# Kernel tuning notes

Measured on AMD Instinct MI355X. Metric: run time of the kernel, lower is better.

The kernel has to match this reference:

```python
import jax, jax.numpy as jnp
import numpy as np

N = 8192  # source points
M = 8192  # target points
T = 8     # RL path steps


def setup_inputs() -> dict:
    key = jax.random.key(0)
    ks = jax.random.split(key, 6)
    return {
        "source": jax.random.normal(ks[0], (N, 3), jnp.float32),
        "target": jax.random.normal(ks[1], (M, 3), jnp.float32),
        "label": jax.random.uniform(ks[2], (N,), jnp.float32),
        "trans_m": 0.01 * jax.random.normal(ks[3], (T, N, 3), jnp.float32),
        "path_m": jax.random.uniform(ks[4], (T, N), jnp.float32),
        "path_maxprob_m": jax.random.uniform(ks[5], (T, N), jnp.float32, minval=0.05, maxval=1.0),
    }


def _catculate_loss2(p1, p2):
    # p1: [N,3], p2: [M,3] -> pairwise squared distances [N,M]
    dist = jnp.sum((p1[:, None, :] - p2[None, :, :]) ** 2, axis=-1)
    dist_min = jnp.min(dist, axis=-1)
    dist_max = jnp.max(dist, axis=-1)
    return 0.99 * dist_min + 0.01 * dist_max  # [N]


def reference(source, target, label, trans_m, path_m, path_maxprob_m):
    p = 0.002
    L0 = 0.4
    lammda = 0.05
    gamma = 0.99
    Tn = path_m.shape[0]

    trans_end = trans_m[-1]
    points_denoise = source - trans_end
    loss_start = _catculate_loss2(source, target)
    loss_end = _catculate_loss2(points_denoise, target)
    loss_dt = loss_end - loss_start

    d = jnp.minimum(loss_end / L0, 1.0)  # where(d>1, 1, d)
    l = jnp.exp(-label)

    reward_end = -p * path_m[-1] - (d + lammda * l) * loss_dt  # [N]
    # rewards: [N, T] = per-step path penalties then final reward
    rewards = jnp.concatenate([(-p * path_m[:-1]).T, reward_end[:, None]], axis=-1)

    logp = jnp.log(path_maxprob_m)  # [T, N]

    # discounted return scan, iterating i = T-1 .. 0
    def step(carry, xs):
        R, L = carry
        lp, r = xs
        R = gamma * R + lp * (r + 0.02)
        return (R, L - R), None

    init = (jnp.zeros_like(reward_end), jnp.zeros_like(reward_end))
    (_, L), _ = jax.lax.scan(step, init, (logp[::-1], rewards.T[::-1]))
    loss = L / Tn  # [N]
    return jnp.mean(loss)
```

## Files before the change

### kernel.cpp

```cpp
#include <hip/hip_runtime.h>
#include <math.h>

#define TPB 256
#define TILE 128

__global__ __launch_bounds__(TPB) void k1_partial_minmax(
    const float* __restrict__ source,
    const float* __restrict__ target,
    const float* __restrict__ trans_m,
    float4* __restrict__ part,
    int* __restrict__ counter,
    int N, int M, int T, int S)
{
    if (blockIdx.x == 0 && blockIdx.y == 0 && threadIdx.x == 0) *counter = 0;

    const int chunk = M / S;
    const int i = blockIdx.x * TPB + threadIdx.x;
    const int s = blockIdx.y;

    __shared__ float4 tgt[TILE];

    const float sx = source[i * 3 + 0];
    const float sy = source[i * 3 + 1];
    const float sz = source[i * 3 + 2];
    const long teoff = (long)(T - 1) * N * 3 + (long)i * 3;
    const float ex = sx - trans_m[teoff + 0];
    const float ey = sy - trans_m[teoff + 1];
    const float ez = sz - trans_m[teoff + 2];

    const float ss = fmaf(sx, sx, fmaf(sy, sy, sz * sz));
    const float ee = fmaf(ex, ex, fmaf(ey, ey, ez * ez));
    const float vsx = -2.0f * sx, vsy = -2.0f * sy, vsz = -2.0f * sz;
    const float vex = -2.0f * ex, vey = -2.0f * ey, vez = -2.0f * ez;

    float mins = 3.402823e38f, maxs = -3.402823e38f;
    float mine = 3.402823e38f, maxe = -3.402823e38f;

    const int t_begin = s * chunk;
    const int t_end   = t_begin + chunk;

    for (int t0 = t_begin; t0 < t_end; t0 += TILE) {
        __syncthreads();
        for (int j = threadIdx.x; j < TILE; j += TPB) {
            const float tx = target[(long)(t0 + j) * 3 + 0];
            const float ty = target[(long)(t0 + j) * 3 + 1];
            const float tz = target[(long)(t0 + j) * 3 + 2];
            const float q  = fmaf(tx, tx, fmaf(ty, ty, tz * tz));
            tgt[j] = make_float4(tx, ty, tz, q);
        }
        __syncthreads();

        #pragma unroll 8
        for (int j = 0; j < TILE; ++j) {
            const float4 t = tgt[j];
            float a = fmaf(vsx, t.x, t.w);
            a = fmaf(vsy, t.y, a);
            a = fmaf(vsz, t.z, a);
            mins = fminf(mins, a);
            maxs = fmaxf(maxs, a);
            float b = fmaf(vex, t.x, t.w);
            b = fmaf(vey, t.y, b);
            b = fmaf(vez, t.z, b);
            mine = fminf(mine, b);
            maxe = fmaxf(maxe, b);
        }
    }

    part[(long)s * N + i] = make_float4(mins + ss, maxs + ss, mine + ee, maxe + ee);
}

__global__ __launch_bounds__(TPB) void k2_loss(
    const float4* __restrict__ part,
    const float* __restrict__ label,
    const float* __restrict__ path_m,
    const float* __restrict__ path_maxprob_m,
    float* __restrict__ blocksums,
    int* __restrict__ counter,
    float* __restrict__ out,
    int N, int S, int T)
{
    const int i = blockIdx.x * TPB + threadIdx.x;

    float mins = 3.402823e38f, maxs = -3.402823e38f;
    float mine = 3.402823e38f, maxe = -3.402823e38f;
    #pragma unroll 4
    for (int s = 0; s < S; ++s) {
        const float4 v = part[(long)s * N + i];
        mins = fminf(mins, v.x);
        maxs = fmaxf(maxs, v.y);
        mine = fminf(mine, v.z);
        maxe = fmaxf(maxe, v.w);
    }

    const float p = 0.002f, L0 = 0.4f, lam = 0.05f, gamma = 0.99f;
    const float loss_start = 0.99f * mins + 0.01f * maxs;
    const float loss_end   = 0.99f * mine + 0.01f * maxe;
    const float loss_dt    = loss_end - loss_start;
    const float d = fminf(loss_end / L0, 1.0f);
    const float l = expf(-label[i]);
    const float reward_end = -p * path_m[(long)(T - 1) * N + i]
                             - (d + lam * l) * loss_dt;

    float R = 0.0f, L = 0.0f;
    for (int t = T - 1; t >= 0; --t) {
        const float r  = (t == T - 1) ? reward_end
                                      : (-p * path_m[(long)t * N + i]);
        const float lp = logf(path_maxprob_m[(long)t * N + i]);
        R = gamma * R + lp * (r + 0.02f);
        L -= R;
    }
    float v = L / (float)T;

    for (int off = 32; off > 0; off >>= 1) v += __shfl_down(v, off, 64);
    __shared__ float red[TPB / 64];
    __shared__ bool amLast;
    const int wid = threadIdx.x >> 6, lane = threadIdx.x & 63;
    if (lane == 0) red[wid] = v;
    __syncthreads();
    if (threadIdx.x == 0) {
        float t = 0.0f;
        #pragma unroll
        for (int w = 0; w < TPB / 64; ++w) t += red[w];
        blocksums[blockIdx.x] = t;
        __threadfence();
        const int old = atomicAdd(counter, 1);
        amLast = (old == (int)gridDim.x - 1);
    }
    __syncthreads();
    if (amLast && threadIdx.x == 0) {
        __threadfence();
        float tot = 0.0f;
        for (int b = 0; b < (int)gridDim.x; ++b)
            tot += ((volatile float*)blocksums)[b];
        out[0] = tot / (float)N;
    }
}

extern "C" void kernel_launch(void* const* d_in, const int* in_sizes, int n_in,
                              void* d_out, int out_size, void* d_ws, size_t ws_size,
                              hipStream_t stream) {
    const float* source = (const float*)d_in[0];
    const float* target = (const float*)d_in[1];
    const float* label  = (const float*)d_in[2];
    const float* trans  = (const float*)d_in[3];
    const float* path   = (const float*)d_in[4];
    const float* pmax   = (const float*)d_in[5];

    const int N = in_sizes[0] / 3;
    const int M = in_sizes[1] / 3;
    const int T = in_sizes[3] / (N * 3);
    const int nbx = N / TPB;

    int S = 64;
    while (S > 1 && ((size_t)S * N * sizeof(float4)
                         + (size_t)(nbx + 1) * sizeof(float) > ws_size
                     || (M / S) < TILE))
        S >>= 1;

    float4* part     = (float4*)d_ws;
    float* blocksums = (float*)(part + (size_t)S * N);
    int*   counter   = (int*)(blocksums + nbx);

    k1_partial_minmax<<<dim3(nbx, S), TPB, 0, stream>>>(
        source, target, trans, part, counter, N, M, T, S);
    k2_loss<<<nbx, TPB, 0, stream>>>(
        part, label, path, pmax, blocksums, counter, (float*)d_out, N, S, T);
}
```

Before: 88.26 us.

## Fuse min/max and loss kernels via per-column last-block counters, two points per thread

Merges the pairwise min/max pass and the per-point loss/reduction into one kernel. The last block to finish each column of target slices, found with a device-global atomic counter, does the loss. Each thread now handles two source points to reuse each shared-memory target load, and S is fixed to M/TILE (64 slices of 128 targets), which removes the ws-size check. This drops a kernel launch and the gap between kernels. In exchange it relies on device-global counters that reset themselves and on a threadfence-based handoff, and it no longer checks that the partial buffer fits in the workspace.

```diff
diff --git a/kernel.cpp b/kernel.cpp
--- a/kernel.cpp
+++ b/kernel.cpp
@@ -3,95 +3,28 @@
 
 #define TPB 256
 #define TILE 128
+#define PPT 2
+#define MAXCOL 64
 
-__global__ __launch_bounds__(TPB) void k1_partial_minmax(
-    const float* __restrict__ source,
-    const float* __restrict__ target,
-    const float* __restrict__ trans_m,
-    float4* __restrict__ part,
-    int* __restrict__ counter,
-    int N, int M, int T, int S)
-{
-    if (blockIdx.x == 0 && blockIdx.y == 0 && threadIdx.x == 0) *counter = 0;
+__device__ int   g_colcnt[MAXCOL];
+__device__ int   g_fincnt;
+__device__ float g_colsum[MAXCOL];
 
-    const int chunk = M / S;
-    const int i = blockIdx.x * TPB + threadIdx.x;
-    const int s = blockIdx.y;
-
-    __shared__ float4 tgt[TILE];
-
-    const float sx = source[i * 3 + 0];
-    const float sy = source[i * 3 + 1];
-    const float sz = source[i * 3 + 2];
-    const long teoff = (long)(T - 1) * N * 3 + (long)i * 3;
-    const float ex = sx - trans_m[teoff + 0];
-    const float ey = sy - trans_m[teoff + 1];
-    const float ez = sz - trans_m[teoff + 2];
-
-    const float ss = fmaf(sx, sx, fmaf(sy, sy, sz * sz));
-    const float ee = fmaf(ex, ex, fmaf(ey, ey, ez * ez));
-    const float vsx = -2.0f * sx, vsy = -2.0f * sy, vsz = -2.0f * sz;
-    const float vex = -2.0f * ex, vey = -2.0f * ey, vez = -2.0f * ez;
-
-    float mins = 3.402823e38f, maxs = -3.402823e38f;
-    float mine = 3.402823e38f, maxe = -3.402823e38f;
-
-    const int t_begin = s * chunk;
-    const int t_end   = t_begin + chunk;
-
-    for (int t0 = t_begin; t0 < t_end; t0 += TILE) {
-        __syncthreads();
-        for (int j = threadIdx.x; j < TILE; j += TPB) {
-            const float tx = target[(long)(t0 + j) * 3 + 0];
-            const float ty = target[(long)(t0 + j) * 3 + 1];
-            const float tz = target[(long)(t0 + j) * 3 + 2];
-            const float q  = fmaf(tx, tx, fmaf(ty, ty, tz * tz));
-            tgt[j] = make_float4(tx, ty, tz, q);
-        }
-        __syncthreads();
-
-        #pragma unroll 8
-        for (int j = 0; j < TILE; ++j) {
-            const float4 t = tgt[j];
-            float a = fmaf(vsx, t.x, t.w);
-            a = fmaf(vsy, t.y, a);
-            a = fmaf(vsz, t.z, a);
-            mins = fminf(mins, a);
-            maxs = fmaxf(maxs, a);
-            float b = fmaf(vex, t.x, t.w);
-            b = fmaf(vey, t.y, b);
-            b = fmaf(vez, t.z, b);
-            mine = fminf(mine, b);
-            maxe = fmaxf(maxe, b);
-        }
-    }
-
-    part[(long)s * N + i] = make_float4(mins + ss, maxs + ss, mine + ee, maxe + ee);
-}
-
-__global__ __launch_bounds__(TPB) void k2_loss(
+__device__ __forceinline__ float point_loss(
     const float4* __restrict__ part,
     const float* __restrict__ label,
     const float* __restrict__ path_m,
     const float* __restrict__ path_maxprob_m,
-    float* __restrict__ blocksums,
-    int* __restrict__ counter,
-    float* __restrict__ out,
-    int N, int S, int T)
+    int i, int N, int S, int T)
 {
-    const int i = blockIdx.x * TPB + threadIdx.x;
-
     float mins = 3.402823e38f, maxs = -3.402823e38f;
     float mine = 3.402823e38f, maxe = -3.402823e38f;
     #pragma unroll 4
     for (int s = 0; s < S; ++s) {
         const float4 v = part[(long)s * N + i];
-        mins = fminf(mins, v.x);
-        maxs = fmaxf(maxs, v.y);
-        mine = fminf(mine, v.z);
-        maxe = fmaxf(maxe, v.w);
+        mins = fminf(mins, v.x); maxs = fmaxf(maxs, v.y);
+        mine = fminf(mine, v.z); maxe = fmaxf(maxe, v.w);
     }
-
     const float p = 0.002f, L0 = 0.4f, lam = 0.05f, gamma = 0.99f;
     const float loss_start = 0.99f * mins + 0.01f * maxs;
     const float loss_end   = 0.99f * mine + 0.01f * maxe;
@@ -100,7 +33,6 @@
     const float l = expf(-label[i]);
     const float reward_end = -p * path_m[(long)(T - 1) * N + i]
                              - (d + lam * l) * loss_dt;
-
     float R = 0.0f, L = 0.0f;
     for (int t = T - 1; t >= 0; --t) {
         const float r  = (t == T - 1) ? reward_end
@@ -109,30 +41,110 @@
         R = gamma * R + lp * (r + 0.02f);
         L -= R;
     }
-    float v = L / (float)T;
+    return L / (float)T;
+}
+
+__global__ __launch_bounds__(TPB) void fused_reward(
+    const float* __restrict__ source,
+    const float* __restrict__ target,
+    const float* __restrict__ label,
+    const float* __restrict__ trans_m,
+    const float* __restrict__ path_m,
+    const float* __restrict__ path_maxprob_m,
+    float4* __restrict__ part,
+    float* __restrict__ out,
+    int N, int M, int T, int S, int NB)
+{
+    const int bx  = blockIdx.x;
+    const int s   = blockIdx.y;
+    const int tid = threadIdx.x;
+
+    __shared__ float4 tgt[TILE];
+
+    if (tid < TILE) {
+        const long j = (long)s * TILE + tid;
+        const float tx = target[j * 3 + 0];
+        const float ty = target[j * 3 + 1];
+        const float tz = target[j * 3 + 2];
+        tgt[tid] = make_float4(tx, ty, tz, fmaf(tx, tx, fmaf(ty, ty, tz * tz)));
+    }
+
+    const int i0 = bx * (PPT * TPB) + tid;
+    const int i1 = i0 + TPB;
+
+    float sx0 = source[i0 * 3 + 0], sy0 = source[i0 * 3 + 1], sz0 = source[i0 * 3 + 2];
+    float sx1 = source[i1 * 3 + 0], sy1 = source[i1 * 3 + 1], sz1 = source[i1 * 3 + 2];
+    const long te = (long)(T - 1) * N * 3;
+    const float ex0 = sx0 - trans_m[te + (long)i0 * 3 + 0];
+    const float ey0 = sy0 - trans_m[te + (long)i0 * 3 + 1];
+    const float ez0 = sz0 - trans_m[te + (long)i0 * 3 + 2];
+    const float ex1 = sx1 - trans_m[te + (long)i1 * 3 + 0];
+    const float ey1 = sy1 - trans_m[te + (long)i1 * 3 + 1];
+    const float ez1 = sz1 - trans_m[te + (long)i1 * 3 + 2];
+
+    const float ss0 = fmaf(sx0, sx0, fmaf(sy0, sy0, sz0 * sz0));
+    const float ss1 = fmaf(sx1, sx1, fmaf(sy1, sy1, sz1 * sz1));
+    const float ee0 = fmaf(ex0, ex0, fmaf(ey0, ey0, ez0 * ez0));
+    const float ee1 = fmaf(ex1, ex1, fmaf(ey1, ey1, ez1 * ez1));
+    sx0 *= -2.0f; sy0 *= -2.0f; sz0 *= -2.0f;
+    sx1 *= -2.0f; sy1 *= -2.0f; sz1 *= -2.0f;
+    const float fx0 = -2.0f * ex0, fy0 = -2.0f * ey0, fz0 = -2.0f * ez0;
+    const float fx1 = -2.0f * ex1, fy1 = -2.0f * ey1, fz1 = -2.0f * ez1;
+
+    float mn_s0 = 3.402823e38f, mx_s0 = -3.402823e38f;
+    float mn_e0 = 3.402823e38f, mx_e0 = -3.402823e38f;
+    float mn_s1 = 3.402823e38f, mx_s1 = -3.402823e38f;
+    float mn_e1 = 3.402823e38f, mx_e1 = -3.402823e38f;
+
+    __syncthreads();
+
+    #pragma unroll 8
+    for (int j = 0; j < TILE; ++j) {
+        const float4 t = tgt[j];
+        float a0 = fmaf(sx0, t.x, t.w); a0 = fmaf(sy0, t.y, a0); a0 = fmaf(sz0, t.z, a0);
+        mn_s0 = fminf(mn_s0, a0); mx_s0 = fmaxf(mx_s0, a0);
+        float b0 = fmaf(fx0, t.x, t.w); b0 = fmaf(fy0, t.y, b0); b0 = fmaf(fz0, t.z, b0);
+        mn_e0 = fminf(mn_e0, b0); mx_e0 = fmaxf(mx_e0, b0);
+        float a1 = fmaf(sx1, t.x, t.w); a1 = fmaf(sy1, t.y, a1); a1 = fmaf(sz1, t.z, a1);
+        mn_s1 = fminf(mn_s1, a1); mx_s1 = fmaxf(mx_s1, a1);
+        float b1 = fmaf(fx1, t.x, t.w); b1 = fmaf(fy1, t.y, b1); b1 = fmaf(fz1, t.z, b1);
+        mn_e1 = fminf(mn_e1, b1); mx_e1 = fmaxf(mx_e1, b1);
+    }
+
+    part[(long)s * N + i0] = make_float4(mn_s0 + ss0, mx_s0 + ss0, mn_e0 + ee0, mx_e0 + ee0);
+    part[(long)s * N + i1] = make_float4(mn_s1 + ss1, mx_s1 + ss1, mn_e1 + ee1, mx_e1 + ee1);
+
+    __threadfence();
+    __shared__ int s_old;
+    if (tid == 0) s_old = atomicAdd(&g_colcnt[bx], 1);
+    __syncthreads();
+    if (s_old != S - 1) return;
+    if (tid == 0) g_colcnt[bx] = 0;
+    __threadfence();
+
+    float v = point_loss(part, label, path_m, path_maxprob_m, i0, N, S, T)
+            + point_loss(part, label, path_m, path_maxprob_m, i1, N, S, T);
 
     for (int off = 32; off > 0; off >>= 1) v += __shfl_down(v, off, 64);
     __shared__ float red[TPB / 64];
-    __shared__ bool amLast;
-    const int wid = threadIdx.x >> 6, lane = threadIdx.x & 63;
+    const int wid = tid >> 6, lane = tid & 63;
     if (lane == 0) red[wid] = v;
     __syncthreads();
-    if (threadIdx.x == 0) {
-        float t = 0.0f;
+    if (tid == 0) {
+        float csum = 0.0f;
         #pragma unroll
-        for (int w = 0; w < TPB / 64; ++w) t += red[w];
-        blocksums[blockIdx.x] = t;
+        for (int w = 0; w < TPB / 64; ++w) csum += red[w];
+        g_colsum[bx] = csum;
         __threadfence();
-        const int old = atomicAdd(counter, 1);
-        amLast = (old == (int)gridDim.x - 1);
-    }
-    __syncthreads();
-    if (amLast && threadIdx.x == 0) {
-        __threadfence();
-        float tot = 0.0f;
-        for (int b = 0; b < (int)gridDim.x; ++b)
-            tot += ((volatile float*)blocksums)[b];
-        out[0] = tot / (float)N;
+        const int o2 = atomicAdd(&g_fincnt, 1);
+        if (o2 == NB - 1) {
+            g_fincnt = 0;
+            __threadfence();
+            float tot = 0.0f;
+            for (int b = 0; b < NB; ++b)
+                tot += ((volatile float*)g_colsum)[b];
+            out[0] = tot / (float)N;
+        }
     }
 }
 
@@ -149,20 +161,12 @@
     const int N = in_sizes[0] / 3;
     const int M = in_sizes[1] / 3;
     const int T = in_sizes[3] / (N * 3);
-    const int nbx = N / TPB;
+    const int S  = M / TILE;
+    const int NB = N / (PPT * TPB);
 
-    int S = 64;
-    while (S > 1 && ((size_t)S * N * sizeof(float4)
-                         + (size_t)(nbx + 1) * sizeof(float) > ws_size
-                     || (M / S) < TILE))
-        S >>= 1;
+    float4* part = (float4*)d_ws;
 
-    float4* part     = (float4*)d_ws;
-    float* blocksums = (float*)(part + (size_t)S * N);
-    int*   counter   = (int*)(blocksums + nbx);
-
-    k1_partial_minmax<<<dim3(nbx, S), TPB, 0, stream>>>(
-        source, target, trans, part, counter, N, M, T, S);
-    k2_loss<<<nbx, TPB, 0, stream>>>(
-        part, label, path, pmax, blocksums, counter, (float*)d_out, N, S, T);
+    fused_reward<<<dim3(NB, S), TPB, 0, stream>>>(
+        source, target, label, trans, path, pmax,
+        part, (float*)d_out, N, M, T, S, NB);
 }
```

Measured after the change: 177.5 us. +101.1%, slower.

## Process two source points per thread with packed f32x2 target math

Applied to the files above, without the earlier changes.

Each thread now handles two source points and processes two targets per iteration, using 2-wide float vectors so the compiler can emit packed FMA and min/max instructions. Shared memory switches from float4 per target to SoA f32x2 arrays, so each LDS read now serves four point-target combinations instead of one. The grid for the first kernel is halved along x. The cost is higher register pressure and fewer blocks, which may lower occupancy.

```diff
diff --git a/kernel.cpp b/kernel.cpp
--- a/kernel.cpp
+++ b/kernel.cpp
@@ -3,6 +3,9 @@
 
 #define TPB 256
 #define TILE 128
+#define PPT 2
+
+typedef float f32x2 __attribute__((ext_vector_type(2)));
 
 __global__ __launch_bounds__(TPB) void k1_partial_minmax(
     const float* __restrict__ source,
@@ -15,58 +18,82 @@
     if (blockIdx.x == 0 && blockIdx.y == 0 && threadIdx.x == 0) *counter = 0;
 
     const int chunk = M / S;
-    const int i = blockIdx.x * TPB + threadIdx.x;
-    const int s = blockIdx.y;
+    const int bx  = blockIdx.x;
+    const int s   = blockIdx.y;
+    const int tid = threadIdx.x;
 
-    __shared__ float4 tgt[TILE];
+    __shared__ f32x2 s_tx[TILE / 2], s_ty[TILE / 2], s_tz[TILE / 2], s_tw[TILE / 2];
 
-    const float sx = source[i * 3 + 0];
-    const float sy = source[i * 3 + 1];
-    const float sz = source[i * 3 + 2];
-    const long teoff = (long)(T - 1) * N * 3 + (long)i * 3;
-    const float ex = sx - trans_m[teoff + 0];
-    const float ey = sy - trans_m[teoff + 1];
-    const float ez = sz - trans_m[teoff + 2];
+    const int i0 = bx * (PPT * TPB) + tid;
+    const int i1 = i0 + TPB;
 
-    const float ss = fmaf(sx, sx, fmaf(sy, sy, sz * sz));
-    const float ee = fmaf(ex, ex, fmaf(ey, ey, ez * ez));
-    const float vsx = -2.0f * sx, vsy = -2.0f * sy, vsz = -2.0f * sz;
-    const float vex = -2.0f * ex, vey = -2.0f * ey, vez = -2.0f * ez;
+    float sx0 = source[i0 * 3 + 0], sy0 = source[i0 * 3 + 1], sz0 = source[i0 * 3 + 2];
+    float sx1 = source[i1 * 3 + 0], sy1 = source[i1 * 3 + 1], sz1 = source[i1 * 3 + 2];
+    const long te = (long)(T - 1) * N * 3;
+    const float ex0 = sx0 - trans_m[te + (long)i0 * 3 + 0];
+    const float ey0 = sy0 - trans_m[te + (long)i0 * 3 + 1];
+    const float ez0 = sz0 - trans_m[te + (long)i0 * 3 + 2];
+    const float ex1 = sx1 - trans_m[te + (long)i1 * 3 + 0];
+    const float ey1 = sy1 - trans_m[te + (long)i1 * 3 + 1];
+    const float ez1 = sz1 - trans_m[te + (long)i1 * 3 + 2];
 
-    float mins = 3.402823e38f, maxs = -3.402823e38f;
-    float mine = 3.402823e38f, maxe = -3.402823e38f;
+    const float ss0 = fmaf(sx0, sx0, fmaf(sy0, sy0, sz0 * sz0));
+    const float ss1 = fmaf(sx1, sx1, fmaf(sy1, sy1, sz1 * sz1));
+    const float ee0 = fmaf(ex0, ex0, fmaf(ey0, ey0, ez0 * ez0));
+    const float ee1 = fmaf(ex1, ex1, fmaf(ey1, ey1, ez1 * ez1));
+
+    const f32x2 a0x = (f32x2)(-2.0f * sx0), a0y = (f32x2)(-2.0f * sy0), a0z = (f32x2)(-2.0f * sz0);
+    const f32x2 a1x = (f32x2)(-2.0f * sx1), a1y = (f32x2)(-2.0f * sy1), a1z = (f32x2)(-2.0f * sz1);
+    const f32x2 b0x = (f32x2)(-2.0f * ex0), b0y = (f32x2)(-2.0f * ey0), b0z = (f32x2)(-2.0f * ez0);
+    const f32x2 b1x = (f32x2)(-2.0f * ex1), b1y = (f32x2)(-2.0f * ey1), b1z = (f32x2)(-2.0f * ez1);
+
+    const f32x2 INF = (f32x2)(3.402823e38f), NINF = (f32x2)(-3.402823e38f);
+    f32x2 mn_s0 = INF, mx_s0 = NINF, mn_e0 = INF, mx_e0 = NINF;
+    f32x2 mn_s1 = INF, mx_s1 = NINF, mn_e1 = INF, mx_e1 = NINF;
 
     const int t_begin = s * chunk;
     const int t_end   = t_begin + chunk;
 
     for (int t0 = t_begin; t0 < t_end; t0 += TILE) {
         __syncthreads();
-        for (int j = threadIdx.x; j < TILE; j += TPB) {
-            const float tx = target[(long)(t0 + j) * 3 + 0];
-            const float ty = target[(long)(t0 + j) * 3 + 1];
-            const float tz = target[(long)(t0 + j) * 3 + 2];
-            const float q  = fmaf(tx, tx, fmaf(ty, ty, tz * tz));
-            tgt[j] = make_float4(tx, ty, tz, q);
+        if (tid < TILE) {
+            const long j = (long)t0 + tid;
+            const float tx = target[j * 3 + 0];
+            const float ty = target[j * 3 + 1];
+            const float tz = target[j * 3 + 2];
+            ((float*)s_tx)[tid] = tx;
+            ((float*)s_ty)[tid] = ty;
+            ((float*)s_tz)[tid] = tz;
+            ((float*)s_tw)[tid] = fmaf(tx, tx, fmaf(ty, ty, tz * tz));
         }
         __syncthreads();
 
         #pragma unroll 8
-        for (int j = 0; j < TILE; ++j) {
-            const float4 t = tgt[j];
-            float a = fmaf(vsx, t.x, t.w);
-            a = fmaf(vsy, t.y, a);
-            a = fmaf(vsz, t.z, a);
-            mins = fminf(mins, a);
-            maxs = fmaxf(maxs, a);
-            float b = fmaf(vex, t.x, t.w);
-            b = fmaf(vey, t.y, b);
-            b = fmaf(vez, t.z, b);
-            mine = fminf(mine, b);
-            maxe = fmaxf(maxe, b);
+        for (int j2 = 0; j2 < TILE / 2; ++j2) {
+            const f32x2 tx = s_tx[j2], ty = s_ty[j2], tz = s_tz[j2], tw = s_tw[j2];
+            f32x2 a = a0x * tx + tw;  a = a0y * ty + a;  a = a0z * tz + a;
+            mn_s0 = __builtin_elementwise_min(mn_s0, a);
+            mx_s0 = __builtin_elementwise_max(mx_s0, a);
+            f32x2 b = b0x * tx + tw;  b = b0y * ty + b;  b = b0z * tz + b;
+            mn_e0 = __builtin_elementwise_min(mn_e0, b);
+            mx_e0 = __builtin_elementwise_max(mx_e0, b);
+            f32x2 c = a1x * tx + tw;  c = a1y * ty + c;  c = a1z * tz + c;
+            mn_s1 = __builtin_elementwise_min(mn_s1, c);
+            mx_s1 = __builtin_elementwise_max(mx_s1, c);
+            f32x2 d = b1x * tx + tw;  d = b1y * ty + d;  d = b1z * tz + d;
+            mn_e1 = __builtin_elementwise_min(mn_e1, d);
+            mx_e1 = __builtin_elementwise_max(mx_e1, d);
         }
     }
 
-    part[(long)s * N + i] = make_float4(mins + ss, maxs + ss, mine + ee, maxe + ee);
+    part[(long)s * N + i0] = make_float4(fminf(mn_s0.x, mn_s0.y) + ss0,
+                                         fmaxf(mx_s0.x, mx_s0.y) + ss0,
+                                         fminf(mn_e0.x, mn_e0.y) + ee0,
+                                         fmaxf(mx_e0.x, mx_e0.y) + ee0);
+    part[(long)s * N + i1] = make_float4(fminf(mn_s1.x, mn_s1.y) + ss1,
+                                         fmaxf(mx_s1.x, mx_s1.y) + ss1,
+                                         fminf(mn_e1.x, mn_e1.y) + ee1,
+                                         fmaxf(mx_e1.x, mx_e1.y) + ee1);
 }
 
 __global__ __launch_bounds__(TPB) void k2_loss(
@@ -149,20 +176,21 @@
     const int N = in_sizes[0] / 3;
     const int M = in_sizes[1] / 3;
     const int T = in_sizes[3] / (N * 3);
-    const int nbx = N / TPB;
+    const int nbx1 = N / (PPT * TPB);
+    const int nbx2 = N / TPB;
 
     int S = 64;
     while (S > 1 && ((size_t)S * N * sizeof(float4)
-                         + (size_t)(nbx + 1) * sizeof(float) > ws_size
+                         + (size_t)(nbx2 + 1) * sizeof(float) > ws_size
                      || (M / S) < TILE))
         S >>= 1;
 
     float4* part     = (float4*)d_ws;
     float* blocksums = (float*)(part + (size_t)S * N);
-    int*   counter   = (int*)(blocksums + nbx);
+    int*   counter   = (int*)(blocksums + nbx2);
 
-    k1_partial_minmax<<<dim3(nbx, S), TPB, 0, stream>>>(
+    k1_partial_minmax<<<dim3(nbx1, S), TPB, 0, stream>>>(
         source, target, trans, part, counter, N, M, T, S);
-    k2_loss<<<nbx, TPB, 0, stream>>>(
+    k2_loss<<<nbx2, TPB, 0, stream>>>(
         part, label, path, pmax, blocksums, counter, (float*)d_out, N, S, T);
 }
```

After: 91.74 us. 4.0% more time.
